# Kernel tuning notes

Hardware: AMD Instinct MI355X
Metric: run time of the kernel (lower is better)

## Reference

```python
import jax, jax.numpy as jnp
import numpy as np

ITERS = 3

def squash(x, axis=-1):
    norm = jnp.linalg.norm(x, axis=axis, keepdims=True)
    scale = norm ** 2 / (1 + norm ** 2) / (norm + 1e-08)
    return scale * x

def setup_inputs() -> dict:
    key = jax.random.key(0)
    kx, kw = jax.random.split(key)
    x = jax.random.normal(kx, (64, 8000, 8), dtype=jnp.float32)
    W = 0.01 * jax.random.normal(kw, (10, 8000, 16, 8), dtype=jnp.float32)
    return {"x": x, "W": W}

def reference(x, W):
    # u_hat[b,o,i,d] = W[o,i,d,e] @ x[b,i,e]
    u_hat = jnp.einsum('oide,bie->boid', W, x)  # [B, O, I, D]
    temp_u_hat = jax.lax.stop_gradient(u_hat)
    B, O, I, D = u_hat.shape
    b = jnp.zeros((B, O, I, 1), dtype=u_hat.dtype)
    v = jnp.ones((B, O, D), dtype=u_hat.dtype)
    for i in range(ITERS):
        c = jax.nn.softmax(b, axis=1)  # over out_caps
        if i < ITERS - 1:
            s = (c * temp_u_hat).sum(axis=2)       # [B, O, D]
            v = squash(s)
            # agreement: u_hat . v over dim D
            b = b + jnp.einsum('boid,bod->boi', temp_u_hat, v)[..., None]
        else:
            s = (c * u_hat).sum(axis=2)
            v = squash(s)
    return v
```

## Files before the change

### kernel.cpp

```cpp
#include <hip/hip_runtime.h>
#include <hip/hip_fp16.h>
#include <math.h>

#define IN 8000
#define OC 10
#define NUNIT 1000
#define VACC_F (64 * OC * 16)
#define PART_H (64 * OC * 16)

#define REC_B   28672
#define REC_H   14336
#define XOFF_B  20480
#define XOFF_H  10240
#define REC_TOTAL_B ((size_t)NUNIT * REC_B)

typedef __fp16 h2 __attribute__((ext_vector_type(2)));
typedef _Float16 half8 __attribute__((ext_vector_type(8)));
typedef float f32x16 __attribute__((ext_vector_type(16)));

__device__ __forceinline__ h2 asb(unsigned int v) { return __builtin_bit_cast(h2, v); }

__device__ __forceinline__ float dot2(h2 a, h2 b, float c) {
#if __has_builtin(__builtin_amdgcn_fdot2)
    return __builtin_amdgcn_fdot2(a, b, c, false);
#else
    return fmaf((float)a[0], (float)b[0], fmaf((float)a[1], (float)b[1], c));
#endif
}

__device__ __forceinline__ unsigned int pk_rn(float a, float b) {
    return __builtin_bit_cast(unsigned int, __float22half2_rn(make_float2(a, b)));
}

#define GLDS16(gp, lp) __builtin_amdgcn_global_load_lds(                      \
    (const __attribute__((address_space(1))) void*)(gp),                      \
    (__attribute__((address_space(3))) void*)(lp), 16, 0, 0)

__global__ __launch_bounds__(256) void caps_prep(
    const float* __restrict__ W, const float* __restrict__ x,
    __fp16* __restrict__ rec)
{
    const int t   = threadIdx.x;
    const int blk = blockIdx.x;
    if (blk < 1250) {
        const int gt = blk * 256 + t;
#pragma unroll
        for (int k = 0; k < 4; ++k) {
            int g  = gt + k * 320000;
            int u  = g / 1280;
            int r  = g - u * 1280;
            int il = r / 160;
            int rr = r - il * 160;
            int o  = rr >> 4;
            int d  = rr & 15;
            const float* ip = W + ((size_t)o * IN + (size_t)(u * 8 + il)) * 128 + d * 8;
            float4 f0 = *(const float4*)(ip);
            float4 f1 = *(const float4*)(ip + 4);
            uint4 pk = make_uint4(pk_rn(f0.x, f0.y), pk_rn(f0.z, f0.w),
                                  pk_rn(f1.x, f1.y), pk_rn(f1.z, f1.w));
            *(uint4*)(rec + (size_t)u * REC_H + il * 1280 + o * 128 + d * 8) = pk;
        }
    } else {
        const int u    = (blk - 1250) * 4 + (t >> 6);
        const int lane = t & 63;
#pragma unroll
        for (int il = 0; il < 8; ++il) {
            const float* ip = x + ((size_t)lane * IN + (size_t)(u * 8 + il)) * 8;
            float4 f0 = *(const float4*)(ip);
            float4 f1 = *(const float4*)(ip + 4);
            uint4 pk = make_uint4(pk_rn(f0.x, f0.y), pk_rn(f0.z, f0.w),
                                  pk_rn(f1.x, f1.y), pk_rn(f1.z, f1.w));
            *(uint4*)(rec + (size_t)u * REC_H + XOFF_H + il * 512 + lane * 8) = pk;
        }
    }
}

template<int UNIFORM>
__global__ __launch_bounds__(256, 2) void caps_pass(
    const __fp16* __restrict__ rec, const float* __restrict__ Vacc,
    __fp16* __restrict__ part)
{
    __shared__ __align__(16) unsigned char sm[2 * REC_B];
    __shared__ __align__(16) unsigned char zs[16];

    const int t    = threadIdx.x;
    const int w    = t >> 6;
    const int lane = t & 63;
    const int lo   = lane & 31;
    const int hi   = lane >> 5;
    const int bt   = w & 1;
    const int ph   = w >> 1;
    const int b    = bt * 32 + lo;

    if (t < 4) ((unsigned int*)zs)[t] = 0u;

    h2 vh[10][4];
    if (!UNIFORM) {
        const float* vp = Vacc + (size_t)b * (OC * 16);
        const float L2E = 1.44269504f;
#pragma unroll
        for (int o = 0; o < OC; ++o) {
            float4 fa = *(const float4*)(vp + o * 16 + 4 * hi);
            float4 fb = *(const float4*)(vp + o * 16 + 8 + 4 * hi);
            vh[o][0] = asb(pk_rn(fa.x * L2E, fa.y * L2E));
            vh[o][1] = asb(pk_rn(fa.z * L2E, fa.w * L2E));
            vh[o][2] = asb(pk_rn(fb.x * L2E, fb.y * L2E));
            vh[o][3] = asb(pk_rn(fb.z * L2E, fb.w * L2E));
        }
    }

    f32x16 acc[5];
    h2 acch[5][8];
    if (UNIFORM) {
#pragma unroll
        for (int op = 0; op < 5; ++op)
#pragma unroll
            for (int k = 0; k < 16; ++k) acc[op][k] = 0.f;
    } else {
#pragma unroll
        for (int op = 0; op < 5; ++op)
#pragma unroll
            for (int q = 0; q < 8; ++q) acch[op][q] = h2{(__fp16)0.f, (__fp16)0.f};
    }

    f32x16 zc;
#pragma unroll
    for (int k = 0; k < 16; ++k) zc[k] = 0.f;

    const int bid  = blockIdx.x;
    const int grid = gridDim.x;

    auto issue = [&](int st, int bufi) {
        const char* g = (const char*)rec + (size_t)st * REC_B + (size_t)lane * 16;
        unsigned char* lb = sm + bufi * REC_B;
#pragma unroll
        for (int c = 0; c < 7; ++c) {
            const int q = c * 4 + w;
            GLDS16(g + q * 1024, lb + q * 1024);
        }
    };

    issue(bid, 0);
    if (bid + grid < NUNIT) issue(bid + grid, 1);
    __syncthreads();

    int cur = 0;
    for (int st = bid; st < NUNIT; st += grid) {
        const unsigned char* buf = sm + cur * REC_B;

        if (UNIFORM) {
#pragma unroll
            for (int ip = 0; ip < 2; ++ip) {
                const int il0 = ph * 4 + ip * 2;
                half8 xb = *(const half8*)(buf + XOFF_B + (il0 + hi) * 1024 + b * 16);
#pragma unroll
                for (int op = 0; op < 5; ++op) {
                    half8 av = *(const half8*)(buf + (il0 + hi) * 2560 + op * 512 + lo * 16);
                    acc[op] = __builtin_amdgcn_mfma_f32_32x32x16_f16(av, xb, acc[op], 0, 0, 0);
                }
            }
        } else {
#pragma unroll 1
            for (int u = 0; u < 4; ++u) {
                const int il = ph * 4 + u;
                const unsigned char* xaddr = (lane < 32)
                    ? (buf + XOFF_B + il * 1024 + b * 16)
                    : (const unsigned char*)zs;
                half8 xb = *(const half8*)xaddr;

                h2 uh2[5][8];
                float lgf[10];
#pragma unroll
                for (int op = 0; op < 5; ++op) {
                    half8 av = *(const half8*)(buf + il * 2560 + op * 512 + lo * 16);
                    f32x16 C = __builtin_amdgcn_mfma_f32_32x32x16_f16(av, xb, zc, 0, 0, 0);
#pragma unroll
                    for (int q = 0; q < 8; ++q)
                        uh2[op][q] = __builtin_amdgcn_cvt_pkrtz(C[2 * q], C[2 * q + 1]);
                    float l0 = 0.f, l1 = 0.f;
#pragma unroll
                    for (int qq = 0; qq < 4; ++qq) {
                        l0 = dot2(uh2[op][qq],     vh[op * 2][qq],     l0);
                        l1 = dot2(uh2[op][4 + qq], vh[op * 2 + 1][qq], l1);
                    }
                    lgf[op * 2]     = l0;
                    lgf[op * 2 + 1] = l1;
                }
#pragma unroll
                for (int pp = 0; pp < 5; ++pp) {
                    h2 lp = asb(pk_rn(lgf[2 * pp], lgf[2 * pp + 1]));
                    int ob = __shfl_xor(__builtin_bit_cast(int, lp), 32);
                    h2 s2 = lp + __builtin_bit_cast(h2, ob);
                    lgf[2 * pp]     = (float)s2[0];
                    lgf[2 * pp + 1] = (float)s2[1];
                }
                float m0 = fmaxf(fmaxf(lgf[0], lgf[1]), lgf[2]);
                float m1 = fmaxf(fmaxf(lgf[3], lgf[4]), lgf[5]);
                float m2 = fmaxf(fmaxf(lgf[6], lgf[7]), lgf[8]);
                float mx = fmaxf(fmaxf(m0, m1), fmaxf(m2, lgf[9]));
                float pe[10];
#pragma unroll
                for (int o = 0; o < OC; ++o)
                    pe[o] = __builtin_amdgcn_exp2f(lgf[o] - mx);
                float s01 = pe[0] + pe[1], s23 = pe[2] + pe[3];
                float s45 = pe[4] + pe[5], s67 = pe[6] + pe[7];
                float s89 = pe[8] + pe[9];
                float se = ((s01 + s23) + (s45 + s67)) + s89;
                float rs = __builtin_amdgcn_rcpf(se);
#pragma unroll
                for (int op = 0; op < 5; ++op) {
                    float c0 = pe[op * 2] * rs;
                    float c1 = pe[op * 2 + 1] * rs;
                    h2 ch0 = __builtin_amdgcn_cvt_pkrtz(c0, c0);
                    h2 ch1 = __builtin_amdgcn_cvt_pkrtz(c1, c1);
#pragma unroll
                    for (int q = 0; q < 4; ++q) {
                        acch[op][q]     = ch0 * uh2[op][q]     + acch[op][q];
                        acch[op][4 + q] = ch1 * uh2[op][4 + q] + acch[op][4 + q];
                    }
                }
            }
        }

        const int nxt = st + 2 * grid;
        if (nxt < NUNIT) {
            __syncthreads();
            issue(nxt, cur);
            __syncthreads();
        }
        cur ^= 1;
    }

    float* red = (float*)sm;
#pragma unroll 1
    for (int phase = 0; phase < 2; ++phase) {
        __syncthreads();
        if (ph == phase) {
#pragma unroll
            for (int op = 0; op < 5; ++op)
#pragma unroll
                for (int q = 0; q < 8; ++q) {
                    const int o  = op * 2 + (q >> 2);
                    const int d0 = 2 * (q & 1) + 8 * ((q >> 1) & 1) + 4 * hi;
                    float e0, e1;
                    if (UNIFORM) { e0 = acc[op][2 * q]; e1 = acc[op][2 * q + 1]; }
                    else         { e0 = (float)acch[op][q][0]; e1 = (float)acch[op][q][1]; }
                    float* p = &red[(size_t)b * 164 + o * 16 + d0];
                    if (phase == 0) {
                        *(float2*)p = make_float2(e0, e1);
                    } else {
                        float2 v2 = *(const float2*)p;
                        v2.x += e0; v2.y += e1;
                        *(float2*)p = v2;
                    }
                }
        }
    }
    __syncthreads();
    unsigned int* dst = (unsigned int*)part;
    for (int q = t; q < PART_H / 2; q += 256) {
        int bo = q >> 3;
        int u8 = q & 7;
        int bb = bo / 10;
        int oo = bo - bb * 10;
        float2 v2 = *(const float2*)&red[(size_t)bb * 164 + oo * 16 + u8 * 2];
        dst[(size_t)(bo * grid + bid) * 8 + u8] = pk_rn(v2.x, v2.y);
    }
}

__global__ __launch_bounds__(256) void caps_reduce(
    const __fp16* __restrict__ part, float* __restrict__ Vacc,
    float* __restrict__ out, int nchunk, int mode, float scale)
{
    const int bo = blockIdx.x;
    const int t  = threadIdx.x;
    const int d2 = t & 3;
    const int s  = t >> 2;

    const unsigned int* p32 = (const unsigned int*)part + (size_t)bo * nchunk * 8;
    float4 a = make_float4(0.f, 0.f, 0.f, 0.f);
    for (int c = s; c < nchunk; c += 64) {
        uint2 v = *(const uint2*)(p32 + (size_t)c * 8 + d2 * 2);
        h2 lov = asb(v.x), hiv = asb(v.y);
        a.x += (float)lov[0]; a.y += (float)lov[1];
        a.z += (float)hiv[0]; a.w += (float)hiv[1];
    }
#pragma unroll
    for (int m = 4; m <= 32; m <<= 1) {
        a.x += __shfl_xor(a.x, m); a.y += __shfl_xor(a.y, m);
        a.z += __shfl_xor(a.z, m); a.w += __shfl_xor(a.w, m);
    }
    __shared__ float red[4][16];
    const int wv = t >> 6;
    if ((t & 63) < 4) {
        red[wv][d2 * 4 + 0] = a.x; red[wv][d2 * 4 + 1] = a.y;
        red[wv][d2 * 4 + 2] = a.z; red[wv][d2 * 4 + 3] = a.w;
    }
    __syncthreads();
    if (t < 16) {
        float sv = (red[0][t] + red[1][t] + red[2][t] + red[3][t]) * scale;
        float n2 = sv * sv;
#pragma unroll
        for (int m = 1; m < 16; m <<= 1) n2 += __shfl_xor(n2, m);
        float norm = sqrtf(n2);
        float scl  = n2 / (1.f + n2) / (norm + 1e-8f);
        float v = scl * sv;
        if (mode == 2)      out[bo * 16 + t] = v;
        else if (mode == 0) Vacc[bo * 16 + t] = v;
        else                Vacc[bo * 16 + t] += v;
    }
}

extern "C" void kernel_launch(void* const* d_in, const int* in_sizes, int n_in,
                              void* d_out, int out_size, void* d_ws, size_t ws_size,
                              hipStream_t stream) {
    const float* x = (const float*)d_in[0];
    const float* W = (const float*)d_in[1];
    float* out = (float*)d_out;

    char* ws = (char*)d_ws;
    float*  Vacc = (float*)ws;
    __fp16* rec  = (__fp16*)(ws + VACC_F * sizeof(float));
    __fp16* part = (__fp16*)(ws + VACC_F * sizeof(float) + REC_TOTAL_B);

    size_t head = VACC_F * sizeof(float) + REC_TOTAL_B;
    size_t avail = (ws_size > head) ? ws_size - head : 0;
    long slots = (long)(avail / (PART_H * sizeof(__fp16)));
    int grid = (int)((slots < 500) ? slots : 500);
    if (grid < 1) grid = 1;

    caps_prep<<<1500, 256, 0, stream>>>(W, x, rec);

    caps_pass<1><<<grid, 256, 0, stream>>>(rec, Vacc, part);
    caps_reduce<<<640, 256, 0, stream>>>(part, Vacc, out, grid, 0, 0.1f);
    caps_pass<0><<<grid, 256, 0, stream>>>(rec, Vacc, part);
    caps_reduce<<<640, 256, 0, stream>>>(part, Vacc, out, grid, 1, 1.0f);
    caps_pass<0><<<grid, 256, 0, stream>>>(rec, Vacc, part);
    caps_reduce<<<640, 256, 0, stream>>>(part, Vacc, out, grid, 2, 1.0f);
}
```

Baseline: 161.6 us.

## Replace partial buffers and reduce kernels with atomic accumulation and fused squash

Each routing pass now atomically adds its per-block 64x160 sums straight into a global fp32 accumulator, instead of writing fp16 partials that a separate reduce kernel later sums. The squash of the previous pass's sums is recomputed inside the next pass's prologue, so the reduce launches go away and the final squash runs in a tiny finishing kernel. The accumulators are zeroed inside the prep kernel. This removes two launches and the round trip through the partial buffer, but adds 500 blocks x 10240 fp32 atomics per pass onto the same addresses. Summation order also becomes nondeterministic.

```diff
diff --git a/kernel.cpp b/kernel.cpp
--- a/kernel.cpp
+++ b/kernel.cpp
@@ -5,9 +5,6 @@
 #define IN 8000
 #define OC 10
 #define NUNIT 1000
-#define VACC_F (64 * OC * 16)
-#define PART_H (64 * OC * 16)
-
 #define REC_B   28672
 #define REC_H   14336
 #define XOFF_B  20480
@@ -38,10 +35,11 @@
 
 __global__ __launch_bounds__(256) void caps_prep(
     const float* __restrict__ W, const float* __restrict__ x,
-    __fp16* __restrict__ rec)
+    __fp16* __restrict__ rec, float* __restrict__ Sall)
 {
     const int t   = threadIdx.x;
     const int blk = blockIdx.x;
+    if (blk < 120) Sall[blk * 256 + t] = 0.f;
     if (blk < 1250) {
         const int gt = blk * 256 + t;
 #pragma unroll
@@ -75,10 +73,10 @@
     }
 }
 
-template<int UNIFORM>
+template<int ITER>
 __global__ __launch_bounds__(256, 2) void caps_pass(
-    const __fp16* __restrict__ rec, const float* __restrict__ Vacc,
-    __fp16* __restrict__ part)
+    const __fp16* __restrict__ rec, const float* __restrict__ S0,
+    const float* __restrict__ S1, float* __restrict__ Sout)
 {
     __shared__ __align__(16) unsigned char sm[2 * REC_B];
     __shared__ __align__(16) unsigned char zs[16];
@@ -95,23 +93,44 @@
     if (t < 4) ((unsigned int*)zs)[t] = 0u;
 
     h2 vh[10][4];
-    if (!UNIFORM) {
-        const float* vp = Vacc + (size_t)b * (OC * 16);
+    if (ITER >= 1) {
         const float L2E = 1.44269504f;
+        const float* s0p = S0 + (size_t)b * 160 + 4 * hi;
+        const float* s1p = S1 + (size_t)b * 160 + 4 * hi;
 #pragma unroll
         for (int o = 0; o < OC; ++o) {
-            float4 fa = *(const float4*)(vp + o * 16 + 4 * hi);
-            float4 fb = *(const float4*)(vp + o * 16 + 8 + 4 * hi);
-            vh[o][0] = asb(pk_rn(fa.x * L2E, fa.y * L2E));
-            vh[o][1] = asb(pk_rn(fa.z * L2E, fa.w * L2E));
-            vh[o][2] = asb(pk_rn(fb.x * L2E, fb.y * L2E));
-            vh[o][3] = asb(pk_rn(fb.z * L2E, fb.w * L2E));
+            float4 a0 = *(const float4*)(s0p + o * 16);
+            float4 a1 = *(const float4*)(s0p + o * 16 + 8);
+            a0.x *= 0.1f; a0.y *= 0.1f; a0.z *= 0.1f; a0.w *= 0.1f;
+            a1.x *= 0.1f; a1.y *= 0.1f; a1.z *= 0.1f; a1.w *= 0.1f;
+            float n2 = a0.x*a0.x + a0.y*a0.y + a0.z*a0.z + a0.w*a0.w
+                     + a1.x*a1.x + a1.y*a1.y + a1.z*a1.z + a1.w*a1.w;
+            n2 += __shfl_xor(n2, 32);
+            float nrm = sqrtf(n2);
+            float scl = n2 / (1.f + n2) / (nrm + 1e-8f);
+            float v0 = scl*a0.x, v1 = scl*a0.y, v2 = scl*a0.z, v3 = scl*a0.w;
+            float v4 = scl*a1.x, v5 = scl*a1.y, v6 = scl*a1.z, v7 = scl*a1.w;
+            if (ITER == 2) {
+                float4 c0 = *(const float4*)(s1p + o * 16);
+                float4 c1 = *(const float4*)(s1p + o * 16 + 8);
+                float m2 = c0.x*c0.x + c0.y*c0.y + c0.z*c0.z + c0.w*c0.w
+                         + c1.x*c1.x + c1.y*c1.y + c1.z*c1.z + c1.w*c1.w;
+                m2 += __shfl_xor(m2, 32);
+                float nr2 = sqrtf(m2);
+                float sc2 = m2 / (1.f + m2) / (nr2 + 1e-8f);
+                v0 += sc2*c0.x; v1 += sc2*c0.y; v2 += sc2*c0.z; v3 += sc2*c0.w;
+                v4 += sc2*c1.x; v5 += sc2*c1.y; v6 += sc2*c1.z; v7 += sc2*c1.w;
+            }
+            vh[o][0] = asb(pk_rn(v0 * L2E, v1 * L2E));
+            vh[o][1] = asb(pk_rn(v2 * L2E, v3 * L2E));
+            vh[o][2] = asb(pk_rn(v4 * L2E, v5 * L2E));
+            vh[o][3] = asb(pk_rn(v6 * L2E, v7 * L2E));
         }
     }
 
     f32x16 acc[5];
     h2 acch[5][8];
-    if (UNIFORM) {
+    if (ITER == 0) {
 #pragma unroll
         for (int op = 0; op < 5; ++op)
 #pragma unroll
@@ -148,7 +167,7 @@
     for (int st = bid; st < NUNIT; st += grid) {
         const unsigned char* buf = sm + cur * REC_B;
 
-        if (UNIFORM) {
+        if (ITER == 0) {
 #pragma unroll
             for (int ip = 0; ip < 2; ++ip) {
                 const int il0 = ph * 4 + ip * 2;
@@ -243,72 +262,33 @@
                     const int o  = op * 2 + (q >> 2);
                     const int d0 = 2 * (q & 1) + 8 * ((q >> 1) & 1) + 4 * hi;
                     float e0, e1;
-                    if (UNIFORM) { e0 = acc[op][2 * q]; e1 = acc[op][2 * q + 1]; }
-                    else         { e0 = (float)acch[op][q][0]; e1 = (float)acch[op][q][1]; }
+                    if (ITER == 0) { e0 = acc[op][2 * q]; e1 = acc[op][2 * q + 1]; }
+                    else           { e0 = (float)acch[op][q][0]; e1 = (float)acch[op][q][1]; }
                     float* p = &red[(size_t)b * 164 + o * 16 + d0];
-                    if (phase == 0) {
-                        *(float2*)p = make_float2(e0, e1);
-                    } else {
-                        float2 v2 = *(const float2*)p;
-                        v2.x += e0; v2.y += e1;
-                        *(float2*)p = v2;
-                    }
+                    if (phase == 0) *(float2*)p = make_float2(e0, e1);
+                    else { float2 v2 = *(const float2*)p; v2.x += e0; v2.y += e1; *(float2*)p = v2; }
                 }
         }
     }
     __syncthreads();
-    unsigned int* dst = (unsigned int*)part;
-    for (int q = t; q < PART_H / 2; q += 256) {
-        int bo = q >> 3;
-        int u8 = q & 7;
-        int bb = bo / 10;
-        int oo = bo - bb * 10;
-        float2 v2 = *(const float2*)&red[(size_t)bb * 164 + oo * 16 + u8 * 2];
-        dst[(size_t)(bo * grid + bid) * 8 + u8] = pk_rn(v2.x, v2.y);
-    }
-}
-
-__global__ __launch_bounds__(256) void caps_reduce(
-    const __fp16* __restrict__ part, float* __restrict__ Vacc,
-    float* __restrict__ out, int nchunk, int mode, float scale)
+    for (int q = t; q < 64 * 160; q += 256) {
+        int bb = q / 160;
+        int r  = q - bb * 160;
+        atomicAdd(&Sout[bb * 160 + r], red[(size_t)bb * 164 + r]);
+    }
+}
+
+__global__ __launch_bounds__(256) void caps_fin(
+    const float* __restrict__ S2, float* __restrict__ out)
 {
-    const int bo = blockIdx.x;
-    const int t  = threadIdx.x;
-    const int d2 = t & 3;
-    const int s  = t >> 2;
-
-    const unsigned int* p32 = (const unsigned int*)part + (size_t)bo * nchunk * 8;
-    float4 a = make_float4(0.f, 0.f, 0.f, 0.f);
-    for (int c = s; c < nchunk; c += 64) {
-        uint2 v = *(const uint2*)(p32 + (size_t)c * 8 + d2 * 2);
-        h2 lov = asb(v.x), hiv = asb(v.y);
-        a.x += (float)lov[0]; a.y += (float)lov[1];
-        a.z += (float)hiv[0]; a.w += (float)hiv[1];
-    }
-#pragma unroll
-    for (int m = 4; m <= 32; m <<= 1) {
-        a.x += __shfl_xor(a.x, m); a.y += __shfl_xor(a.y, m);
-        a.z += __shfl_xor(a.z, m); a.w += __shfl_xor(a.w, m);
-    }
-    __shared__ float red[4][16];
-    const int wv = t >> 6;
-    if ((t & 63) < 4) {
-        red[wv][d2 * 4 + 0] = a.x; red[wv][d2 * 4 + 1] = a.y;
-        red[wv][d2 * 4 + 2] = a.z; red[wv][d2 * 4 + 3] = a.w;
-    }
-    __syncthreads();
-    if (t < 16) {
-        float sv = (red[0][t] + red[1][t] + red[2][t] + red[3][t]) * scale;
-        float n2 = sv * sv;
-#pragma unroll
-        for (int m = 1; m < 16; m <<= 1) n2 += __shfl_xor(n2, m);
-        float norm = sqrtf(n2);
-        float scl  = n2 / (1.f + n2) / (norm + 1e-8f);
-        float v = scl * sv;
-        if (mode == 2)      out[bo * 16 + t] = v;
-        else if (mode == 0) Vacc[bo * 16 + t] = v;
-        else                Vacc[bo * 16 + t] += v;
-    }
+    const int g = blockIdx.x * 256 + threadIdx.x;
+    float sv = S2[g];
+    float n2 = sv * sv;
+#pragma unroll
+    for (int m = 1; m < 16; m <<= 1) n2 += __shfl_xor(n2, m);
+    float nrm = sqrtf(n2);
+    float scl = n2 / (1.f + n2) / (nrm + 1e-8f);
+    out[g] = scl * sv;
 }
 
 extern "C" void kernel_launch(void* const* d_in, const int* in_sizes, int n_in,
@@ -319,22 +299,17 @@
     float* out = (float*)d_out;
 
     char* ws = (char*)d_ws;
-    float*  Vacc = (float*)ws;
-    __fp16* rec  = (__fp16*)(ws + VACC_F * sizeof(float));
-    __fp16* part = (__fp16*)(ws + VACC_F * sizeof(float) + REC_TOTAL_B);
-
-    size_t head = VACC_F * sizeof(float) + REC_TOTAL_B;
-    size_t avail = (ws_size > head) ? ws_size - head : 0;
-    long slots = (long)(avail / (PART_H * sizeof(__fp16)));
-    int grid = (int)((slots < 500) ? slots : 500);
-    if (grid < 1) grid = 1;
-
-    caps_prep<<<1500, 256, 0, stream>>>(W, x, rec);
-
-    caps_pass<1><<<grid, 256, 0, stream>>>(rec, Vacc, part);
-    caps_reduce<<<640, 256, 0, stream>>>(part, Vacc, out, grid, 0, 0.1f);
-    caps_pass<0><<<grid, 256, 0, stream>>>(rec, Vacc, part);
-    caps_reduce<<<640, 256, 0, stream>>>(part, Vacc, out, grid, 1, 1.0f);
-    caps_pass<0><<<grid, 256, 0, stream>>>(rec, Vacc, part);
-    caps_reduce<<<640, 256, 0, stream>>>(part, Vacc, out, grid, 2, 1.0f);
-}
+    float* S0 = (float*)ws;
+    float* S1 = S0 + 10240;
+    float* S2 = S1 + 10240;
+    __fp16* rec = (__fp16*)(ws + 3 * 10240 * sizeof(float));
+
+    int grid = 500;
+
+    caps_prep<<<1500, 256, 0, stream>>>(W, x, rec, S0);
+
+    caps_pass<0><<<grid, 256, 0, stream>>>(rec, S0, S1, S0);
+    caps_pass<1><<<grid, 256, 0, stream>>>(rec, S0, S1, S1);
+    caps_pass<2><<<grid, 256, 0, stream>>>(rec, S0, S1, S2);
+    caps_fin<<<40, 256, 0, stream>>>(S2, out);
+}
```

Result: slower. 206.3 us (+27.7%).

## Load x directly into registers and shrink LDS staging to raise occupancy

Applied to the files above, without the earlier changes.

The x portion of each record is now read from global memory straight into registers instead of being staged in LDS. Only the W portion goes through LDS, which shrinks shared memory to about 41KB and lets launch bounds rise to 3 blocks per CU. The double-buffered steady-state loop is replaced by two paths: a special case for exactly two units per block that loads both up front, and a single-buffer fallback with no prefetch overlap. Higher occupancy is meant to hide latency, but the fallback path loses the software pipelining, and register pressure under the tighter bound may cause spills.

```diff
diff --git a/kernel.cpp b/kernel.cpp
--- a/kernel.cpp
+++ b/kernel.cpp
@@ -10,6 +10,7 @@
 
 #define REC_B   28672
 #define REC_H   14336
+#define WREC    20480
 #define XOFF_B  20480
 #define XOFF_H  10240
 #define REC_TOTAL_B ((size_t)NUNIT * REC_B)
@@ -19,6 +20,7 @@
 typedef float f32x16 __attribute__((ext_vector_type(16)));
 
 __device__ __forceinline__ h2 asb(unsigned int v) { return __builtin_bit_cast(h2, v); }
+__device__ __forceinline__ half8 ash8(uint4 v) { return __builtin_bit_cast(half8, v); }
 
 __device__ __forceinline__ float dot2(h2 a, h2 b, float c) {
 #if __has_builtin(__builtin_amdgcn_fdot2)
@@ -76,12 +78,11 @@
 }
 
 template<int UNIFORM>
-__global__ __launch_bounds__(256, 2) void caps_pass(
+__global__ __launch_bounds__(256, 3) void caps_pass(
     const __fp16* __restrict__ rec, const float* __restrict__ Vacc,
     __fp16* __restrict__ part)
 {
-    __shared__ __align__(16) unsigned char sm[2 * REC_B];
-    __shared__ __align__(16) unsigned char zs[16];
+    __shared__ __align__(16) unsigned char sm[41984];
 
     const int t    = threadIdx.x;
     const int w    = t >> 6;
@@ -92,8 +93,6 @@
     const int ph   = w >> 1;
     const int b    = bt * 32 + lo;
 
-    if (t < 4) ((unsigned int*)zs)[t] = 0u;
-
     h2 vh[10][4];
     if (!UNIFORM) {
         const float* vp = Vacc + (size_t)b * (OC * 16);
@@ -132,103 +131,137 @@
 
     auto issue = [&](int st, int bufi) {
         const char* g = (const char*)rec + (size_t)st * REC_B + (size_t)lane * 16;
-        unsigned char* lb = sm + bufi * REC_B;
-#pragma unroll
-        for (int c = 0; c < 7; ++c) {
+        unsigned char* lb = sm + bufi * WREC;
+#pragma unroll
+        for (int c = 0; c < 5; ++c) {
             const int q = c * 4 + w;
             GLDS16(g + q * 1024, lb + q * 1024);
         }
     };
 
-    issue(bid, 0);
-    if (bid + grid < NUNIT) issue(bid + grid, 1);
-    __syncthreads();
-
-    int cur = 0;
-    for (int st = bid; st < NUNIT; st += grid) {
-        const unsigned char* buf = sm + cur * REC_B;
-
+    auto loadx = [&](int st, uint4 (&xq)[4]) {
+        const uint4* xg = (const uint4*)((const char*)rec + (size_t)st * REC_B + XOFF_B);
+#pragma unroll
+        for (int u = 0; u < 4; ++u) {
+            xq[u] = make_uint4(0u, 0u, 0u, 0u);
+            if (lane < 32) xq[u] = xg[(ph * 4 + u) * 64 + b];
+        }
+    };
+    auto loadxu = [&](int st, uint4 (&xq)[2]) {
+        const uint4* xg = (const uint4*)((const char*)rec + (size_t)st * REC_B + XOFF_B);
+#pragma unroll
+        for (int ipp = 0; ipp < 2; ++ipp)
+            xq[ipp] = xg[(ph * 4 + ipp * 2 + hi) * 64 + b];
+    };
+
+    auto proc_u = [&](const unsigned char* buf, uint4 (&xq)[2]) {
+#pragma unroll
+        for (int ipp = 0; ipp < 2; ++ipp) {
+            const int il0 = ph * 4 + ipp * 2;
+            half8 xb = ash8(xq[ipp]);
+#pragma unroll
+            for (int op = 0; op < 5; ++op) {
+                half8 av = *(const half8*)(buf + (il0 + hi) * 2560 + op * 512 + lo * 16);
+                acc[op] = __builtin_amdgcn_mfma_f32_32x32x16_f16(av, xb, acc[op], 0, 0, 0);
+            }
+        }
+    };
+    auto proc_r = [&](const unsigned char* buf, uint4 (&xq)[4]) {
+#pragma unroll 1
+        for (int u = 0; u < 4; ++u) {
+            const int il = ph * 4 + u;
+            half8 xb = ash8(xq[u]);
+
+            h2 uh2[5][8];
+            float lgf[10];
+#pragma unroll
+            for (int op = 0; op < 5; ++op) {
+                half8 av = *(const half8*)(buf + il * 2560 + op * 512 + lo * 16);
+                f32x16 C = __builtin_amdgcn_mfma_f32_32x32x16_f16(av, xb, zc, 0, 0, 0);
+#pragma unroll
+                for (int q = 0; q < 8; ++q)
+                    uh2[op][q] = __builtin_amdgcn_cvt_pkrtz(C[2 * q], C[2 * q + 1]);
+                float l0 = 0.f, l1 = 0.f;
+#pragma unroll
+                for (int qq = 0; qq < 4; ++qq) {
+                    l0 = dot2(uh2[op][qq],     vh[op * 2][qq],     l0);
+                    l1 = dot2(uh2[op][4 + qq], vh[op * 2 + 1][qq], l1);
+                }
+                lgf[op * 2]     = l0;
+                lgf[op * 2 + 1] = l1;
+            }
+#pragma unroll
+            for (int pp = 0; pp < 5; ++pp) {
+                h2 lp = asb(pk_rn(lgf[2 * pp], lgf[2 * pp + 1]));
+                int ob = __shfl_xor(__builtin_bit_cast(int, lp), 32);
+                h2 s2 = lp + __builtin_bit_cast(h2, ob);
+                lgf[2 * pp]     = (float)s2[0];
+                lgf[2 * pp + 1] = (float)s2[1];
+            }
+            float m0 = fmaxf(fmaxf(lgf[0], lgf[1]), lgf[2]);
+            float m1 = fmaxf(fmaxf(lgf[3], lgf[4]), lgf[5]);
+            float m2 = fmaxf(fmaxf(lgf[6], lgf[7]), lgf[8]);
+            float mx = fmaxf(fmaxf(m0, m1), fmaxf(m2, lgf[9]));
+            float pe[10];
+#pragma unroll
+            for (int o = 0; o < OC; ++o)
+                pe[o] = __builtin_amdgcn_exp2f(lgf[o] - mx);
+            float s01 = pe[0] + pe[1], s23 = pe[2] + pe[3];
+            float s45 = pe[4] + pe[5], s67 = pe[6] + pe[7];
+            float s89 = pe[8] + pe[9];
+            float se = ((s01 + s23) + (s45 + s67)) + s89;
+            float rs = __builtin_amdgcn_rcpf(se);
+#pragma unroll
+            for (int op = 0; op < 5; ++op) {
+                float c0 = pe[op * 2] * rs;
+                float c1 = pe[op * 2 + 1] * rs;
+                h2 ch0 = __builtin_amdgcn_cvt_pkrtz(c0, c0);
+                h2 ch1 = __builtin_amdgcn_cvt_pkrtz(c1, c1);
+#pragma unroll
+                for (int q = 0; q < 4; ++q) {
+                    acch[op][q]     = ch0 * uh2[op][q]     + acch[op][q];
+                    acch[op][4 + q] = ch1 * uh2[op][4 + q] + acch[op][4 + q];
+                }
+            }
+        }
+    };
+
+    const int st0 = bid;
+    const int st1 = bid + grid;
+    if (st1 < NUNIT && st0 + 2 * grid >= NUNIT) {
         if (UNIFORM) {
-#pragma unroll
-            for (int ip = 0; ip < 2; ++ip) {
-                const int il0 = ph * 4 + ip * 2;
-                half8 xb = *(const half8*)(buf + XOFF_B + (il0 + hi) * 1024 + b * 16);
-#pragma unroll
-                for (int op = 0; op < 5; ++op) {
-                    half8 av = *(const half8*)(buf + (il0 + hi) * 2560 + op * 512 + lo * 16);
-                    acc[op] = __builtin_amdgcn_mfma_f32_32x32x16_f16(av, xb, acc[op], 0, 0, 0);
-                }
-            }
+            uint4 xa[2], xc[2];
+            loadxu(st0, xa); loadxu(st1, xc);
+            issue(st0, 0);   issue(st1, 1);
+            __syncthreads();
+            proc_u(sm, xa);
+            proc_u(sm + WREC, xc);
         } else {
-#pragma unroll 1
-            for (int u = 0; u < 4; ++u) {
-                const int il = ph * 4 + u;
-                const unsigned char* xaddr = (lane < 32)
-                    ? (buf + XOFF_B + il * 1024 + b * 16)
-                    : (const unsigned char*)zs;
-                half8 xb = *(const half8*)xaddr;
-
-                h2 uh2[5][8];
-                float lgf[10];
-#pragma unroll
-                for (int op = 0; op < 5; ++op) {
-                    half8 av = *(const half8*)(buf + il * 2560 + op * 512 + lo * 16);
-                    f32x16 C = __builtin_amdgcn_mfma_f32_32x32x16_f16(av, xb, zc, 0, 0, 0);
-#pragma unroll
-                    for (int q = 0; q < 8; ++q)
-                        uh2[op][q] = __builtin_amdgcn_cvt_pkrtz(C[2 * q], C[2 * q + 1]);
-                    float l0 = 0.f, l1 = 0.f;
-#pragma unroll
-                    for (int qq = 0; qq < 4; ++qq) {
-                        l0 = dot2(uh2[op][qq],     vh[op * 2][qq],     l0);
-                        l1 = dot2(uh2[op][4 + qq], vh[op * 2 + 1][qq], l1);
-                    }
-                    lgf[op * 2]     = l0;
-                    lgf[op * 2 + 1] = l1;
-                }
-#pragma unroll
-                for (int pp = 0; pp < 5; ++pp) {
-                    h2 lp = asb(pk_rn(lgf[2 * pp], lgf[2 * pp + 1]));
-                    int ob = __shfl_xor(__builtin_bit_cast(int, lp), 32);
-                    h2 s2 = lp + __builtin_bit_cast(h2, ob);
-                    lgf[2 * pp]     = (float)s2[0];
-                    lgf[2 * pp + 1] = (float)s2[1];
-                }
-                float m0 = fmaxf(fmaxf(lgf[0], lgf[1]), lgf[2]);
-                float m1 = fmaxf(fmaxf(lgf[3], lgf[4]), lgf[5]);
-                float m2 = fmaxf(fmaxf(lgf[6], lgf[7]), lgf[8]);
-                float mx = fmaxf(fmaxf(m0, m1), fmaxf(m2, lgf[9]));
-                float pe[10];
-#pragma unroll
-                for (int o = 0; o < OC; ++o)
-                    pe[o] = __builtin_amdgcn_exp2f(lgf[o] - mx);
-                float s01 = pe[0] + pe[1], s23 = pe[2] + pe[3];
-                float s45 = pe[4] + pe[5], s67 = pe[6] + pe[7];
-                float s89 = pe[8] + pe[9];
-                float se = ((s01 + s23) + (s45 + s67)) + s89;
-                float rs = __builtin_amdgcn_rcpf(se);
-#pragma unroll
-                for (int op = 0; op < 5; ++op) {
-                    float c0 = pe[op * 2] * rs;
-                    float c1 = pe[op * 2 + 1] * rs;
-                    h2 ch0 = __builtin_amdgcn_cvt_pkrtz(c0, c0);
-                    h2 ch1 = __builtin_amdgcn_cvt_pkrtz(c1, c1);
-#pragma unroll
-                    for (int q = 0; q < 4; ++q) {
-                        acch[op][q]     = ch0 * uh2[op][q]     + acch[op][q];
-                        acch[op][4 + q] = ch1 * uh2[op][4 + q] + acch[op][4 + q];
-                    }
-                }
-            }
-        }
-
-        const int nxt = st + 2 * grid;
-        if (nxt < NUNIT) {
+            uint4 xa[4], xc[4];
+            loadx(st0, xa); loadx(st1, xc);
+            issue(st0, 0);  issue(st1, 1);
             __syncthreads();
-            issue(nxt, cur);
-            __syncthreads();
-        }
-        cur ^= 1;
+            proc_r(sm, xa);
+            proc_r(sm + WREC, xc);
+        }
+    } else {
+        bool first = true;
+        for (int st = bid; st < NUNIT; st += grid) {
+            if (!first) __syncthreads();
+            issue(st, 0);
+            if (UNIFORM) {
+                uint4 xa[2];
+                loadxu(st, xa);
+                __syncthreads();
+                proc_u(sm, xa);
+            } else {
+                uint4 xa[4];
+                loadx(st, xa);
+                __syncthreads();
+                proc_r(sm, xa);
+            }
+            first = false;
+        }
     }
 
     float* red = (float*)sm;
```

Result: slower. 173.1 us (+7.1%).
